# Performance work log

Measured on AMD Instinct MI355X. Metric: run time of the kernel, lower is better.

Reference implementation:

```python
import jax, jax.numpy as jnp
import numpy as np

B, S, H, L, D, DI = 4, 32, 8, 128, 512, 2048
EPS = 1e-6
TEMP = float(D) ** 0.5


def layer_norm(x, g, b):
    mu = jnp.mean(x, axis=-1, keepdims=True)
    var = jnp.mean((x - mu) ** 2, axis=-1, keepdims=True)
    return (x - mu) * jax.lax.rsqrt(var + EPS) * g + b


def setup_inputs() -> dict:
    key = jax.random.key(0)
    ks = jax.random.split(key, 8)
    x = jax.random.normal(ks[0], (B, S, L, D), jnp.float32)
    mask = jax.random.randint(ks[1], (B, S, L), 0, 2, jnp.int32)
    # learned params
    w = jax.random.normal(ks[2], (1, 1, H, L, D), jnp.float32) * (1.0 / np.sqrt(D))
    v_w = jax.random.normal(ks[3], (D, D), jnp.float32) * 0.02   # nn.Linear weight (out,in)
    ln_g = jnp.ones((D,), jnp.float32)
    ln_b = jnp.zeros((D,), jnp.float32)
    w1 = jax.random.normal(ks[4], (DI, D), jnp.float32) * 0.02
    b1 = jnp.zeros((DI,), jnp.float32)
    w2 = jax.random.normal(ks[5], (D, DI), jnp.float32) * 0.02
    b2 = jnp.zeros((D,), jnp.float32)
    fln_g = jnp.ones((D,), jnp.float32)
    fln_b = jnp.zeros((D,), jnp.float32)
    return {"x": x, "mask": mask, "w": w, "v_w": v_w, "ln_g": ln_g, "ln_b": ln_b,
            "w1": w1, "b1": b1, "w2": w2, "b2": b2, "fln_g": fln_g, "fln_b": fln_b}


def reference(x, mask, w, v_w, ln_g, ln_b, w1, b1, w2, b2, fln_g, fln_b):
    # attn logits: broadcast mul + reduce over d_model == einsum over d
    attn = jnp.einsum('bsld,hld->bshl', x, w[0, 0]) / TEMP           # (B,S,H,L)
    attn = jnp.where(mask[:, :, None, :] == 0, -1e9, attn)
    attn = jax.nn.softmax(attn, axis=-1)                              # dropout: eval mode
    v = jnp.einsum('bsld,ed->bsle', x, v_w)                           # Linear no bias: x @ W.T
    out = jnp.einsum('bsld,bshl->bshd', v, attn)                      # weighted sum readout
    out = layer_norm(out, ln_g, ln_b)
    # PositionwiseFeedForward with residual + LayerNorm
    h = jax.nn.relu(jnp.einsum('bshd,fd->bshf', out, w1) + b1)
    y = jnp.einsum('bshf,df->bshd', h, w2) + b2 + out
    y = layer_norm(y, fln_g, fln_b)
    return y, attn
```

## Files before the change

kernel.cpp:

```cpp
#include <hip/hip_runtime.h>
#include <hip/hip_bf16.h>

#define BB 4
#define SS 32
#define HH 8
#define LL 128
#define DD 512
#define DI 2048
#define EPSN 1e-6f
#define INV_TEMP 0.04419417382415922f

#define NLOGIT_BLK 4096
#define NCAST_GRAN ((DI*DD/4)*2 + (DD*DD/4))
#define NCAST_BLK (NCAST_GRAN / 256)

typedef __attribute__((ext_vector_type(8))) short short8;
typedef __attribute__((ext_vector_type(4))) float float4v;

static __device__ __forceinline__ unsigned short f2b(float f) {
  __hip_bfloat16 h = __float2bfloat16(f);
  return *(unsigned short*)&h;
}

__global__ __launch_bounds__(256) void pre_kernel(
    const float* __restrict__ x, const int* __restrict__ mask,
    const float* __restrict__ w, const float* __restrict__ w1,
    const float* __restrict__ w2, const float* __restrict__ v_w,
    unsigned short* __restrict__ w1b, unsigned short* __restrict__ w2b,
    unsigned short* __restrict__ v_wb, float* __restrict__ logits) {
  int blk = blockIdx.x;
  if (blk < NLOGIT_BLK) {
    int wv = threadIdx.x >> 6, lane = threadIdx.x & 63;
    int p  = blk * 4 + wv;
    int bs = p >> 7, l = p & (LL - 1);

    const float4* xr = (const float4*)(x + ((size_t)bs * LL + l) * DD) + lane * 2;
    float4 x0 = xr[0], x1 = xr[1];

    float acc[HH];
#pragma unroll
    for (int h = 0; h < HH; ++h) {
      const float4* wr = (const float4*)(w + ((size_t)h * LL + l) * DD) + lane * 2;
      float4 w0 = wr[0], w1v = wr[1];
      acc[h] = x0.x * w0.x + x0.y * w0.y + x0.z * w0.z + x0.w * w0.w +
               x1.x * w1v.x + x1.y * w1v.y + x1.z * w1v.z + x1.w * w1v.w;
    }
#pragma unroll
    for (int off = 32; off > 0; off >>= 1) {
#pragma unroll
      for (int h = 0; h < HH; ++h) acc[h] += __shfl_xor(acc[h], off);
    }
    if (lane == 0) {
      int msk = mask[bs * LL + l];
#pragma unroll
      for (int h = 0; h < HH; ++h) {
        float lg = msk ? acc[h] * INV_TEMP : -1e9f;
        logits[((size_t)bs * HH + h) * LL + l] = lg;
      }
    }
  } else {
    const int n1 = (DI * DD) / 4;
    const int n2 = n1;
    int i = (blk - NLOGIT_BLK) * 256 + threadIdx.x;
    const float4* src;
    unsigned short* dst;
    int j = i;
    if (i < n1)           { src = (const float4*)w1;  dst = w1b; }
    else if (i < n1 + n2) { src = (const float4*)w2;  dst = w2b;  j = i - n1; }
    else                  { src = (const float4*)v_w; dst = v_wb; j = i - n1 - n2; }
    float4 v = src[j];
    dst[j * 4 + 0] = f2b(v.x);
    dst[j * 4 + 1] = f2b(v.y);
    dst[j * 4 + 2] = f2b(v.z);
    dst[j * 4 + 3] = f2b(v.w);
  }
}

__global__ __launch_bounds__(256) void xa_kernel(
    const float* __restrict__ x, const float* __restrict__ logits,
    float* __restrict__ attn_out, unsigned short* __restrict__ xab) {
  int bs = blockIdx.x >> 1, half = blockIdx.x & 1;
  int t = threadIdx.x, wv = t >> 6, lane = t & 63;

  __shared__ float sattn_t[LL][HH];

  for (int h = wv; h < HH; h += 4) {
    const float* lg = logits + ((size_t)bs * HH + h) * LL;
    float v0 = lg[lane], v1 = lg[lane + 64];
    float m = fmaxf(v0, v1);
#pragma unroll
    for (int off = 32; off > 0; off >>= 1) m = fmaxf(m, __shfl_xor(m, off));
    float e0 = __expf(v0 - m), e1 = __expf(v1 - m);
    float s = e0 + e1;
#pragma unroll
    for (int off = 32; off > 0; off >>= 1) s += __shfl_xor(s, off);
    float inv = 1.f / s;
    e0 *= inv; e1 *= inv;
    sattn_t[lane][h]      = e0;
    sattn_t[lane + 64][h] = e1;
    if (half == 0) {
      float* ao = attn_out + ((size_t)bs * HH + h) * LL;
      ao[lane]      = e0;
      ao[lane + 64] = e1;
    }
  }
  __syncthreads();

  int e = half * 256 + t;
  const float* xb = x + (size_t)bs * LL * DD;
  float acc[HH];
#pragma unroll
  for (int h = 0; h < HH; ++h) acc[h] = 0.f;
  for (int l = 0; l < LL; ++l) {
    float xv = xb[(size_t)l * DD + e];
    float4 a0 = *(const float4*)&sattn_t[l][0];
    float4 a1 = *(const float4*)&sattn_t[l][4];
    acc[0] += a0.x * xv; acc[1] += a0.y * xv;
    acc[2] += a0.z * xv; acc[3] += a0.w * xv;
    acc[4] += a1.x * xv; acc[5] += a1.y * xv;
    acc[6] += a1.z * xv; acc[7] += a1.w * xv;
  }
  unsigned short* xo = xab + (size_t)bs * HH * DD;
#pragma unroll
  for (int h = 0; h < HH; ++h) xo[h * DD + e] = f2b(acc[h]);
}

__global__ __launch_bounds__(256) void gemm_v_kernel(
    const unsigned short* __restrict__ xab, const unsigned short* __restrict__ v_wb,
    float* __restrict__ out_pre) {
  int blk = blockIdx.x;
  int nt = blk % 8, mt = blk / 8;
  int wv = threadIdx.x >> 6, lane = threadIdx.x & 63;
  int lm = lane & 15, lq = lane >> 4;

  int m0 = mt * 64 + wv * 16;
  int n0 = nt * 64;

  const short8* A0 = (const short8*)(xab + (size_t)(m0 + lm) * DD);
  const short8* Bp[4];
#pragma unroll
  for (int nf = 0; nf < 4; ++nf)
    Bp[nf] = (const short8*)(v_wb + (size_t)(n0 + nf * 16 + lm) * DD);

  float4v acc[4];
#pragma unroll
  for (int nf = 0; nf < 4; ++nf) acc[nf] = (float4v){0.f, 0.f, 0.f, 0.f};

#pragma unroll 2
  for (int ks = 0; ks < DD / 32; ++ks) {
    short8 a0 = A0[ks * 4 + lq];
    short8 b[4];
#pragma unroll
    for (int nf = 0; nf < 4; ++nf) b[nf] = Bp[nf][ks * 4 + lq];
#pragma unroll
    for (int nf = 0; nf < 4; ++nf)
      acc[nf] = __builtin_amdgcn_mfma_f32_16x16x32_bf16(a0, b[nf], acc[nf], 0, 0, 0);
  }

#pragma unroll
  for (int nf = 0; nf < 4; ++nf) {
    int col = n0 + nf * 16 + lm;
#pragma unroll
    for (int r = 0; r < 4; ++r) {
      int row = m0 + lq * 4 + r;
      out_pre[(size_t)row * DD + col] = acc[nf][r];
    }
  }
}

__global__ __launch_bounds__(256) void ln_mid_kernel(
    const float* __restrict__ out_pre, const float* __restrict__ ln_g,
    const float* __restrict__ ln_b, float* __restrict__ o_ln,
    unsigned short* __restrict__ o_lnb) {
  int wv = threadIdx.x >> 6, lane = threadIdx.x & 63;
  int row = blockIdx.x * 4 + wv;

  const float* yp = out_pre + (size_t)row * DD;
  float vals[8];
  float sum = 0.f, sq = 0.f;
#pragma unroll
  for (int k = 0; k < 8; ++k) {
    float v = yp[lane + 64 * k];
    vals[k] = v;
    sum += v;
    sq += v * v;
  }
#pragma unroll
  for (int off = 32; off > 0; off >>= 1) {
    sum += __shfl_xor(sum, off);
    sq  += __shfl_xor(sq, off);
  }
  float mu  = sum * (1.f / DD);
  float var = sq * (1.f / DD) - mu * mu;
  float rs  = rsqrtf(var + EPSN);
  float* op = o_ln + (size_t)row * DD;
  unsigned short* opb = o_lnb + (size_t)row * DD;
#pragma unroll
  for (int k = 0; k < 8; ++k) {
    int d = lane + 64 * k;
    float v = (vals[k] - mu) * rs * ln_g[d] + ln_b[d];
    op[d]  = v;
    opb[d] = f2b(v);
  }
}

__global__ __launch_bounds__(256) void gemm1_kernel(
    const unsigned short* __restrict__ xb, const unsigned short* __restrict__ w1b,
    const float* __restrict__ b1, unsigned short* __restrict__ h1b) {
  int blk = blockIdx.x;
  int nt = blk % 32, mt = blk / 32;
  int wv = threadIdx.x >> 6, lane = threadIdx.x & 63;
  int lm = lane & 15, lq = lane >> 4;

  int m0 = mt * 128 + wv * 32;
  int n0 = nt * 64;

  const short8* A0 = (const short8*)(xb + (size_t)(m0 + lm) * DD);
  const short8* A1 = (const short8*)(xb + (size_t)(m0 + 16 + lm) * DD);
  const short8* Bp[4];
#pragma unroll
  for (int nf = 0; nf < 4; ++nf)
    Bp[nf] = (const short8*)(w1b + (size_t)(n0 + nf * 16 + lm) * DD);

  float4v acc[2][4];
#pragma unroll
  for (int i = 0; i < 2; ++i)
#pragma unroll
    for (int nf = 0; nf < 4; ++nf) acc[i][nf] = (float4v){0.f, 0.f, 0.f, 0.f};

#pragma unroll 2
  for (int ks = 0; ks < DD / 32; ++ks) {
    short8 a0 = A0[ks * 4 + lq];
    short8 a1 = A1[ks * 4 + lq];
    short8 b[4];
#pragma unroll
    for (int nf = 0; nf < 4; ++nf) b[nf] = Bp[nf][ks * 4 + lq];
#pragma unroll
    for (int nf = 0; nf < 4; ++nf) {
      acc[0][nf] = __builtin_amdgcn_mfma_f32_16x16x32_bf16(a0, b[nf], acc[0][nf], 0, 0, 0);
      acc[1][nf] = __builtin_amdgcn_mfma_f32_16x16x32_bf16(a1, b[nf], acc[1][nf], 0, 0, 0);
    }
  }

#pragma unroll
  for (int i = 0; i < 2; ++i)
#pragma unroll
    for (int nf = 0; nf < 4; ++nf) {
      int col = n0 + nf * 16 + lm;
      float bb = b1[col];
#pragma unroll
      for (int r = 0; r < 4; ++r) {
        int row = m0 + i * 16 + lq * 4 + r;
        float v = acc[i][nf][r] + bb;
        h1b[(size_t)row * DI + col] = f2b(fmaxf(v, 0.f));
      }
    }
}

__global__ __launch_bounds__(256) void gemm2_kernel(
    const unsigned short* __restrict__ h1b, const unsigned short* __restrict__ w2b,
    float* __restrict__ y_pre) {
  int blk = blockIdx.x;
  int nt = blk % 8, mt = blk / 8;
  int wv = threadIdx.x >> 6, lane = threadIdx.x & 63;
  int lm = lane & 15, lq = lane >> 4;

  int m0 = mt * 64 + wv * 16;
  int n0 = nt * 64;

  const short8* A0 = (const short8*)(h1b + (size_t)(m0 + lm) * DI);
  const short8* Bp[4];
#pragma unroll
  for (int nf = 0; nf < 4; ++nf)
    Bp[nf] = (const short8*)(w2b + (size_t)(n0 + nf * 16 + lm) * DI);

  float4v acc[4];
#pragma unroll
  for (int nf = 0; nf < 4; ++nf) acc[nf] = (float4v){0.f, 0.f, 0.f, 0.f};

#pragma unroll 2
  for (int ks = 0; ks < DI / 32; ++ks) {
    short8 a0 = A0[ks * 4 + lq];
    short8 b[4];
#pragma unroll
    for (int nf = 0; nf < 4; ++nf) b[nf] = Bp[nf][ks * 4 + lq];
#pragma unroll
    for (int nf = 0; nf < 4; ++nf)
      acc[nf] = __builtin_amdgcn_mfma_f32_16x16x32_bf16(a0, b[nf], acc[nf], 0, 0, 0);
  }

#pragma unroll
  for (int nf = 0; nf < 4; ++nf) {
    int col = n0 + nf * 16 + lm;
#pragma unroll
    for (int r = 0; r < 4; ++r) {
      int row = m0 + lq * 4 + r;
      y_pre[(size_t)row * DD + col] = acc[nf][r];
    }
  }
}

__global__ __launch_bounds__(256) void ln_final_kernel(
    const float* __restrict__ y_pre, const float* __restrict__ o_ln,
    const float* __restrict__ b2, const float* __restrict__ fln_g,
    const float* __restrict__ fln_b, float* __restrict__ y_out) {
  int wv = threadIdx.x >> 6, lane = threadIdx.x & 63;
  int row = blockIdx.x * 4 + wv;

  const float* yp = y_pre + (size_t)row * DD;
  const float* ol = o_ln + (size_t)row * DD;
  float vals[8];
  float sum = 0.f, sq = 0.f;
#pragma unroll
  for (int k = 0; k < 8; ++k) {
    int d = lane + 64 * k;
    float v = yp[d] + b2[d] + ol[d];
    vals[k] = v;
    sum += v;
    sq += v * v;
  }
#pragma unroll
  for (int off = 32; off > 0; off >>= 1) {
    sum += __shfl_xor(sum, off);
    sq  += __shfl_xor(sq, off);
  }
  float mu  = sum * (1.f / DD);
  float var = sq * (1.f / DD) - mu * mu;
  float rs  = rsqrtf(var + EPSN);
  float* yo = y_out + (size_t)row * DD;
#pragma unroll
  for (int k = 0; k < 8; ++k) {
    int d = lane + 64 * k;
    yo[d] = (vals[k] - mu) * rs * fln_g[d] + fln_b[d];
  }
}

extern "C" void kernel_launch(void* const* d_in, const int* in_sizes, int n_in,
                              void* d_out, int out_size, void* d_ws, size_t ws_size,
                              hipStream_t stream) {
  const float* x     = (const float*)d_in[0];
  const int*   mask  = (const int*)d_in[1];
  const float* w     = (const float*)d_in[2];
  const float* v_w   = (const float*)d_in[3];
  const float* ln_g  = (const float*)d_in[4];
  const float* ln_b  = (const float*)d_in[5];
  const float* w1    = (const float*)d_in[6];
  const float* b1    = (const float*)d_in[7];
  const float* w2    = (const float*)d_in[8];
  const float* b2    = (const float*)d_in[9];
  const float* fln_g = (const float*)d_in[10];
  const float* fln_b = (const float*)d_in[11];

  float* y    = (float*)d_out;
  float* attn = y + (size_t)BB * SS * HH * DD;

  char* ws = (char*)d_ws;
  float*          o_ln    = (float*)(ws);
  unsigned short* o_lnb   = (unsigned short*)(ws + 2097152);
  unsigned short* w1b     = (unsigned short*)(ws + 3145728);
  unsigned short* w2b     = (unsigned short*)(ws + 5242880);
  unsigned short* h1b     = (unsigned short*)(ws + 7340032);
  float*          y_pre   = (float*)(ws + 11534336);
  unsigned short* v_wb    = (unsigned short*)(ws + 13631488);
  unsigned short* xab     = (unsigned short*)(ws + 14155776);
  float*          out_pre = (float*)(ws + 15204352);
  float*          logits  = (float*)(ws + 17301504);

  pre_kernel<<<NLOGIT_BLK + NCAST_BLK, 256, 0, stream>>>(
      x, mask, w, w1, w2, v_w, w1b, w2b, v_wb, logits);
  xa_kernel<<<BB * SS * 2, 256, 0, stream>>>(x, logits, attn, xab);
  gemm_v_kernel<<<128, 256, 0, stream>>>(xab, v_wb, out_pre);
  ln_mid_kernel<<<256, 256, 0, stream>>>(out_pre, ln_g, ln_b, o_ln, o_lnb);
  gemm1_kernel<<<256, 256, 0, stream>>>(o_lnb, w1b, b1, h1b);
  gemm2_kernel<<<128, 256, 0, stream>>>(h1b, w2b, y_pre);
  ln_final_kernel<<<256, 256, 0, stream>>>(y_pre, o_ln, b2, fln_g, fln_b, y);
}
```

Before: 186.0 us.

## Split-K the V and FFN2 GEMMs, halve gemm1 tiles, split xa over L

The V-projection and second FFN GEMMs now split the reduction dimension into four slices. Each slice writes an fp32 partial buffer, and the following LayerNorm kernels sum the four slices. gemm1 uses a smaller 64-row tile to double its block count, and the xa kernel uses 512 threads that split the L loop in two and reduce through shared memory. The aim is to fill more compute units on the MI355X, since the earlier grids of 128 or 256 blocks leave many units idle. The cost is extra partial-sum memory traffic and a larger workspace.

```diff
diff --git a/kernel.cpp b/kernel.cpp
--- a/kernel.cpp
+++ b/kernel.cpp
@@ -13,6 +13,9 @@
 #define NLOGIT_BLK 4096
 #define NCAST_GRAN ((DI*DD/4)*2 + (DD*DD/4))
 #define NCAST_BLK (NCAST_GRAN / 256)
+
+#define NROW (BB*SS*HH)
+#define SLICE ((size_t)NROW * DD)
 
 typedef __attribute__((ext_vector_type(8))) short short8;
 typedef __attribute__((ext_vector_type(4))) float float4v;
@@ -76,42 +79,47 @@
   }
 }
 
-__global__ __launch_bounds__(256) void xa_kernel(
+__global__ __launch_bounds__(512) void xa_kernel(
     const float* __restrict__ x, const float* __restrict__ logits,
     float* __restrict__ attn_out, unsigned short* __restrict__ xab) {
   int bs = blockIdx.x >> 1, half = blockIdx.x & 1;
   int t = threadIdx.x, wv = t >> 6, lane = t & 63;
 
   __shared__ float sattn_t[LL][HH];
-
-  for (int h = wv; h < HH; h += 4) {
-    const float* lg = logits + ((size_t)bs * HH + h) * LL;
-    float v0 = lg[lane], v1 = lg[lane + 64];
-    float m = fmaxf(v0, v1);
-#pragma unroll
-    for (int off = 32; off > 0; off >>= 1) m = fmaxf(m, __shfl_xor(m, off));
-    float e0 = __expf(v0 - m), e1 = __expf(v1 - m);
-    float s = e0 + e1;
-#pragma unroll
-    for (int off = 32; off > 0; off >>= 1) s += __shfl_xor(s, off);
-    float inv = 1.f / s;
-    e0 *= inv; e1 *= inv;
-    sattn_t[lane][h]      = e0;
-    sattn_t[lane + 64][h] = e1;
-    if (half == 0) {
-      float* ao = attn_out + ((size_t)bs * HH + h) * LL;
-      ao[lane]      = e0;
-      ao[lane + 64] = e1;
+  __shared__ float sxa[2][HH][256];
+
+  if (wv < 4) {
+    for (int h = wv; h < HH; h += 4) {
+      const float* lg = logits + ((size_t)bs * HH + h) * LL;
+      float v0 = lg[lane], v1 = lg[lane + 64];
+      float m = fmaxf(v0, v1);
+#pragma unroll
+      for (int off = 32; off > 0; off >>= 1) m = fmaxf(m, __shfl_xor(m, off));
+      float e0 = __expf(v0 - m), e1 = __expf(v1 - m);
+      float s = e0 + e1;
+#pragma unroll
+      for (int off = 32; off > 0; off >>= 1) s += __shfl_xor(s, off);
+      float inv = 1.f / s;
+      e0 *= inv; e1 *= inv;
+      sattn_t[lane][h]      = e0;
+      sattn_t[lane + 64][h] = e1;
+      if (half == 0) {
+        float* ao = attn_out + ((size_t)bs * HH + h) * LL;
+        ao[lane]      = e0;
+        ao[lane + 64] = e1;
+      }
     }
   }
   __syncthreads();
 
-  int e = half * 256 + t;
+  int col = t & 255, lseg = t >> 8;
+  int e = half * 256 + col;
   const float* xb = x + (size_t)bs * LL * DD;
   float acc[HH];
 #pragma unroll
   for (int h = 0; h < HH; ++h) acc[h] = 0.f;
-  for (int l = 0; l < LL; ++l) {
+  int l0 = lseg * 64;
+  for (int l = l0; l < l0 + 64; ++l) {
     float xv = xb[(size_t)l * DD + e];
     float4 a0 = *(const float4*)&sattn_t[l][0];
     float4 a1 = *(const float4*)&sattn_t[l][4];
@@ -120,34 +128,41 @@
     acc[4] += a1.x * xv; acc[5] += a1.y * xv;
     acc[6] += a1.z * xv; acc[7] += a1.w * xv;
   }
-  unsigned short* xo = xab + (size_t)bs * HH * DD;
-#pragma unroll
-  for (int h = 0; h < HH; ++h) xo[h * DD + e] = f2b(acc[h]);
+#pragma unroll
+  for (int h = 0; h < HH; ++h) sxa[lseg][h][col] = acc[h];
+  __syncthreads();
+  if (t < 256) {
+    unsigned short* xo = xab + (size_t)bs * HH * DD;
+#pragma unroll
+    for (int h = 0; h < HH; ++h)
+      xo[h * DD + t + half * 256] = f2b(sxa[0][h][t] + sxa[1][h][t]);
+  }
 }
 
 __global__ __launch_bounds__(256) void gemm_v_kernel(
     const unsigned short* __restrict__ xab, const unsigned short* __restrict__ v_wb,
-    float* __restrict__ out_pre) {
+    float* __restrict__ vpart) {
   int blk = blockIdx.x;
-  int nt = blk % 8, mt = blk / 8;
+  int nt = blk & 7, mt = (blk >> 3) & 15, kslice = blk >> 7;
   int wv = threadIdx.x >> 6, lane = threadIdx.x & 63;
   int lm = lane & 15, lq = lane >> 4;
 
   int m0 = mt * 64 + wv * 16;
   int n0 = nt * 64;
-
-  const short8* A0 = (const short8*)(xab + (size_t)(m0 + lm) * DD);
+  int g0 = kslice * 16;
+
+  const short8* A0 = (const short8*)(xab + (size_t)(m0 + lm) * DD) + g0;
   const short8* Bp[4];
 #pragma unroll
   for (int nf = 0; nf < 4; ++nf)
-    Bp[nf] = (const short8*)(v_wb + (size_t)(n0 + nf * 16 + lm) * DD);
+    Bp[nf] = (const short8*)(v_wb + (size_t)(n0 + nf * 16 + lm) * DD) + g0;
 
   float4v acc[4];
 #pragma unroll
   for (int nf = 0; nf < 4; ++nf) acc[nf] = (float4v){0.f, 0.f, 0.f, 0.f};
 
-#pragma unroll 2
-  for (int ks = 0; ks < DD / 32; ++ks) {
+#pragma unroll
+  for (int ks = 0; ks < 4; ++ks) {
     short8 a0 = A0[ks * 4 + lq];
     short8 b[4];
 #pragma unroll
@@ -157,30 +172,32 @@
       acc[nf] = __builtin_amdgcn_mfma_f32_16x16x32_bf16(a0, b[nf], acc[nf], 0, 0, 0);
   }
 
+  float* outp = vpart + (size_t)kslice * SLICE;
 #pragma unroll
   for (int nf = 0; nf < 4; ++nf) {
     int col = n0 + nf * 16 + lm;
 #pragma unroll
     for (int r = 0; r < 4; ++r) {
       int row = m0 + lq * 4 + r;
-      out_pre[(size_t)row * DD + col] = acc[nf][r];
+      outp[(size_t)row * DD + col] = acc[nf][r];
     }
   }
 }
 
 __global__ __launch_bounds__(256) void ln_mid_kernel(
-    const float* __restrict__ out_pre, const float* __restrict__ ln_g,
+    const float* __restrict__ vpart, const float* __restrict__ ln_g,
     const float* __restrict__ ln_b, float* __restrict__ o_ln,
     unsigned short* __restrict__ o_lnb) {
   int wv = threadIdx.x >> 6, lane = threadIdx.x & 63;
   int row = blockIdx.x * 4 + wv;
 
-  const float* yp = out_pre + (size_t)row * DD;
+  const float* p0 = vpart + (size_t)row * DD;
   float vals[8];
   float sum = 0.f, sq = 0.f;
 #pragma unroll
   for (int k = 0; k < 8; ++k) {
-    float v = yp[lane + 64 * k];
+    int d = lane + 64 * k;
+    float v = p0[d] + p0[SLICE + d] + p0[2 * SLICE + d] + p0[3 * SLICE + d];
     vals[k] = v;
     sum += v;
     sq += v * v;
@@ -208,78 +225,71 @@
     const unsigned short* __restrict__ xb, const unsigned short* __restrict__ w1b,
     const float* __restrict__ b1, unsigned short* __restrict__ h1b) {
   int blk = blockIdx.x;
-  int nt = blk % 32, mt = blk / 32;
+  int nt = blk & 31, mt = blk >> 5;
   int wv = threadIdx.x >> 6, lane = threadIdx.x & 63;
   int lm = lane & 15, lq = lane >> 4;
 
-  int m0 = mt * 128 + wv * 32;
+  int m0 = mt * 64 + wv * 16;
   int n0 = nt * 64;
 
   const short8* A0 = (const short8*)(xb + (size_t)(m0 + lm) * DD);
-  const short8* A1 = (const short8*)(xb + (size_t)(m0 + 16 + lm) * DD);
   const short8* Bp[4];
 #pragma unroll
   for (int nf = 0; nf < 4; ++nf)
     Bp[nf] = (const short8*)(w1b + (size_t)(n0 + nf * 16 + lm) * DD);
 
-  float4v acc[2][4];
-#pragma unroll
-  for (int i = 0; i < 2; ++i)
-#pragma unroll
-    for (int nf = 0; nf < 4; ++nf) acc[i][nf] = (float4v){0.f, 0.f, 0.f, 0.f};
-
-#pragma unroll 2
+  float4v acc[4];
+#pragma unroll
+  for (int nf = 0; nf < 4; ++nf) acc[nf] = (float4v){0.f, 0.f, 0.f, 0.f};
+
+#pragma unroll 4
   for (int ks = 0; ks < DD / 32; ++ks) {
     short8 a0 = A0[ks * 4 + lq];
-    short8 a1 = A1[ks * 4 + lq];
     short8 b[4];
 #pragma unroll
     for (int nf = 0; nf < 4; ++nf) b[nf] = Bp[nf][ks * 4 + lq];
 #pragma unroll
-    for (int nf = 0; nf < 4; ++nf) {
-      acc[0][nf] = __builtin_amdgcn_mfma_f32_16x16x32_bf16(a0, b[nf], acc[0][nf], 0, 0, 0);
-      acc[1][nf] = __builtin_amdgcn_mfma_f32_16x16x32_bf16(a1, b[nf], acc[1][nf], 0, 0, 0);
-    }
-  }
-
-#pragma unroll
-  for (int i = 0; i < 2; ++i)
-#pragma unroll
-    for (int nf = 0; nf < 4; ++nf) {
-      int col = n0 + nf * 16 + lm;
-      float bb = b1[col];
-#pragma unroll
-      for (int r = 0; r < 4; ++r) {
-        int row = m0 + i * 16 + lq * 4 + r;
-        float v = acc[i][nf][r] + bb;
-        h1b[(size_t)row * DI + col] = f2b(fmaxf(v, 0.f));
-      }
-    }
+    for (int nf = 0; nf < 4; ++nf)
+      acc[nf] = __builtin_amdgcn_mfma_f32_16x16x32_bf16(a0, b[nf], acc[nf], 0, 0, 0);
+  }
+
+#pragma unroll
+  for (int nf = 0; nf < 4; ++nf) {
+    int col = n0 + nf * 16 + lm;
+    float bb = b1[col];
+#pragma unroll
+    for (int r = 0; r < 4; ++r) {
+      int row = m0 + lq * 4 + r;
+      float v = acc[nf][r] + bb;
+      h1b[(size_t)row * DI + col] = f2b(fmaxf(v, 0.f));
+    }
+  }
 }
 
 __global__ __launch_bounds__(256) void gemm2_kernel(
     const unsigned short* __restrict__ h1b, const unsigned short* __restrict__ w2b,
-    float* __restrict__ y_pre) {
+    float* __restrict__ ypart) {
   int blk = blockIdx.x;
-  int nt = blk % 8, mt = blk / 8;
+  int nt = blk & 7, mt = (blk >> 3) & 15, kslice = blk >> 7;
   int wv = threadIdx.x >> 6, lane = threadIdx.x & 63;
   int lm = lane & 15, lq = lane >> 4;
 
   int m0 = mt * 64 + wv * 16;
   int n0 = nt * 64;
-
-  const short8* A0 = (const short8*)(h1b + (size_t)(m0 + lm) * DI);
+  int g0 = kslice * 64;
+
+  const short8* A0 = (const short8*)(h1b + (size_t)(m0 + lm) * DI) + g0;
   const short8* Bp[4];
 #pragma unroll
   for (int nf = 0; nf < 4; ++nf)
-    Bp[nf] = (const short8*)(w2b + (size_t)(n0 + nf * 16 + lm) * DI);
+    Bp[nf] = (const short8*)(w2b + (size_t)(n0 + nf * 16 + lm) * DI) + g0;
 
   float4v acc[4];
 #pragma unroll
   for (int nf = 0; nf < 4; ++nf) acc[nf] = (float4v){0.f, 0.f, 0.f, 0.f};
 
-#pragma unroll 2
-  for (int ks = 0; ks < DI / 32; ++ks) {
+#pragma unroll 4
+  for (int ks = 0; ks < 16; ++ks) {
     short8 a0 = A0[ks * 4 + lq];
     short8 b[4];
 #pragma unroll
@@ -289,32 +299,34 @@
       acc[nf] = __builtin_amdgcn_mfma_f32_16x16x32_bf16(a0, b[nf], acc[nf], 0, 0, 0);
   }
 
+  float* outp = ypart + (size_t)kslice * SLICE;
 #pragma unroll
   for (int nf = 0; nf < 4; ++nf) {
     int col = n0 + nf * 16 + lm;
 #pragma unroll
     for (int r = 0; r < 4; ++r) {
       int row = m0 + lq * 4 + r;
-      y_pre[(size_t)row * DD + col] = acc[nf][r];
+      outp[(size_t)row * DD + col] = acc[nf][r];
     }
   }
 }
 
 __global__ __launch_bounds__(256) void ln_final_kernel(
-    const float* __restrict__ y_pre, const float* __restrict__ o_ln,
+    const float* __restrict__ ypart, const float* __restrict__ o_ln,
     const float* __restrict__ b2, const float* __restrict__ fln_g,
     const float* __restrict__ fln_b, float* __restrict__ y_out) {
   int wv = threadIdx.x >> 6, lane = threadIdx.x & 63;
   int row = blockIdx.x * 4 + wv;
 
-  const float* yp = y_pre + (size_t)row * DD;
+  const float* p0 = ypart + (size_t)row * DD;
   const float* ol = o_ln + (size_t)row * DD;
   float vals[8];
   float sum = 0.f, sq = 0.f;
 #pragma unroll
   for (int k = 0; k < 8; ++k) {
     int d = lane + 64 * k;
-    float v = yp[d] + b2[d] + ol[d];
+    float v = p0[d] + p0[SLICE + d] + p0[2 * SLICE + d] + p0[3 * SLICE + d] +
+              b2[d] + ol[d];
     vals[k] = v;
     sum += v;
     sq += v * v;
@@ -360,18 +372,18 @@
   unsigned short* w1b     = (unsigned short*)(ws + 3145728);
   unsigned short* w2b     = (unsigned short*)(ws + 5242880);
   unsigned short* h1b     = (unsigned short*)(ws + 7340032);
-  float*          y_pre   = (float*)(ws + 11534336);
-  unsigned short* v_wb    = (unsigned short*)(ws + 13631488);
-  unsigned short* xab     = (unsigned short*)(ws + 14155776);
-  float*          out_pre = (float*)(ws + 15204352);
-  float*          logits  = (float*)(ws + 17301504);
+  float*          ypart   = (float*)(ws + 11534336);
+  unsigned short* v_wb    = (unsigned short*)(ws + 19922944);
+  unsigned short* xab     = (unsigned short*)(ws + 20447232);
+  float*          vpart   = (float*)(ws + 21495808);
+  float*          logits  = (float*)(ws + 29884416);
 
   pre_kernel<<<NLOGIT_BLK + NCAST_BLK, 256, 0, stream>>>(
       x, mask, w, w1, w2, v_w, w1b, w2b, v_wb, logits);
-  xa_kernel<<<BB * SS * 2, 256, 0, stream>>>(x, logits, attn, xab);
-  gemm_v_kernel<<<128, 256, 0, stream>>>(xab, v_wb, out_pre);
-  ln_mid_kernel<<<256, 256, 0, stream>>>(out_pre, ln_g, ln_b, o_ln, o_lnb);
-  gemm1_kernel<<<256, 256, 0, stream>>>(o_lnb, w1b, b1, h1b);
-  gemm2_kernel<<<128, 256, 0, stream>>>(h1b, w2b, y_pre);
-  ln_final_kernel<<<256, 256, 0, stream>>>(y_pre, o_ln, b2, fln_g, fln_b, y);
-}
+  xa_kernel<<<BB * SS * 2, 512, 0, stream>>>(x, logits, attn, xab);
+  gemm_v_kernel<<<512, 256, 0, stream>>>(xab, v_wb, vpart);
+  ln_mid_kernel<<<256, 256, 0, stream>>>(vpart, ln_g, ln_b, o_ln, o_lnb);
+  gemm1_kernel<<<512, 256, 0, stream>>>(o_lnb, w1b, b1, h1b);
+  gemm2_kernel<<<512, 256, 0, stream>>>(h1b, w2b, ypart);
+  ln_final_kernel<<<256, 256, 0, stream>>>(ypart, o_ln, b2, fln_g, fln_b, y);
+}
```

After: 172.6 us. 1.08x faster.
